# Kernel tuning notes

Hardware: AMD Instinct MI355X
Metric: run time of the kernel (lower is better)

## Reference

```python
import jax, jax.numpy as jnp
import numpy as np

N = 20000
E = 640000
H, C = 4, 64
L = 3
B = 16
EPS = 1e-5


def setup_inputs() -> dict:
    key = jax.random.key(0)
    ks = jax.random.split(key, 12)
    x = jax.random.normal(ks[0], (N, 256), dtype=jnp.float32)
    edge_index = jax.random.randint(ks[1], (2, E), 0, N, dtype=jnp.int64)
    batch = jnp.sort(jax.random.randint(ks[2], (N,), 0, B, dtype=jnp.int64))
    s = 0.05
    return {
        "x": x,
        "edge_index": edge_index,
        "batch": batch,
        "Wl": jax.random.normal(ks[3], (L, 256, H * C), dtype=jnp.float32) * s,
        "bl": jnp.zeros((L, H * C), dtype=jnp.float32),
        "Wr": jax.random.normal(ks[4], (L, 256, H * C), dtype=jnp.float32) * s,
        "br": jnp.zeros((L, H * C), dtype=jnp.float32),
        "att": jax.random.normal(ks[5], (L, H, C), dtype=jnp.float32) * s,
        "conv_bias": jnp.zeros((L, H * C), dtype=jnp.float32),
        "prelu_a": jnp.full((L,), 0.25, dtype=jnp.float32),
        "norm_w": jnp.ones((H * C,), dtype=jnp.float32),
        "norm_b": jnp.zeros((H * C,), dtype=jnp.float32),
        "norm_alpha": jnp.ones((H * C,), dtype=jnp.float32),
        "fc_W": jax.random.normal(ks[6], (H * C, 128), dtype=jnp.float32) * s,
        "fc_b": jnp.zeros((128,), dtype=jnp.float32),
    }


def graph_norm(h, w, b, alpha):
    # GraphNorm with batch=None: all rows form one segment (as in source forward)
    mean = jnp.mean(h, axis=0, keepdims=True)
    shifted = h - alpha * mean
    var = jnp.mean(shifted * shifted, axis=0, keepdims=True)
    return w * shifted / jnp.sqrt(var + EPS) + b


def gatv2_layer(h, src, dst, Wl, bl, Wr, br, att, bias):
    xl = (h @ Wl + bl).reshape(N, H, C)  # source transform
    xr = (h @ Wr + br).reshape(N, H, C)  # target transform
    m = jax.nn.leaky_relu(xl[src] + xr[dst], negative_slope=0.2)  # [Etot,H,C]
    e = jnp.einsum("ehc,hc->eh", m, att)  # [Etot,H]
    emax = jax.ops.segment_max(e, dst, num_segments=N)  # self-loops guarantee coverage
    ex = jnp.exp(e - emax[dst])
    denom = jax.ops.segment_sum(ex, dst, num_segments=N)
    alpha = ex / denom[dst]
    out = jax.ops.segment_sum(alpha[:, :, None] * xl[src], dst, num_segments=N)
    return out.reshape(N, H * C) + bias


def reference(x, edge_index, batch, Wl, bl, Wr, br, att, conv_bias, prelu_a,
              norm_w, norm_b, norm_alpha, fc_W, fc_b):
    loop = jnp.arange(N, dtype=edge_index.dtype)
    src = jnp.concatenate([edge_index[0], loop])  # add self-loops (PyG default)
    dst = jnp.concatenate([edge_index[1], loop])
    h = x
    for l in range(L):
        h = gatv2_layer(h, src, dst, Wl[l], bl[l], Wr[l], br[l], att[l], conv_bias[l])
        h = graph_norm(h, norm_w, norm_b, norm_alpha)
        h = jnp.where(h >= 0, h, prelu_a[l] * h)  # PReLU; dropout is identity in eval
    pooled = jax.ops.segment_sum(h, batch, num_segments=B)  # global_add_pool
    pooled = graph_norm(pooled, norm_w, norm_b, norm_alpha)  # shared norm reused after pool
    return pooled @ fc_W + fc_b
```

## Files before the change

### kernel.cpp

```cpp
#include <hip/hip_runtime.h>
#include <math.h>

#define N_NODES 20000
#define N_EDGES 640000
#define ETOT (N_EDGES + N_NODES)
#define HC 256
#define NLAYER 3
#define NBATCH 16
#define GEPS 1e-5f
#define NSLOT 64
#define L2E 1.44269504f

typedef unsigned short u16;
typedef unsigned int u32;
typedef __attribute__((ext_vector_type(8))) short short8;
typedef __attribute__((ext_vector_type(4))) float floatx4;

__device__ __forceinline__ u16 f2bf(float f) {
    u32 u = __float_as_uint(f);
    u32 r = (u + 0x7FFFu + ((u >> 16) & 1u)) >> 16;
    return (u16)r;
}

__device__ __forceinline__ float4 bf2f4(uint2 u) {
    float4 r;
    r.x = __uint_as_float(u.x << 16);
    r.y = __uint_as_float(u.x & 0xFFFF0000u);
    r.z = __uint_as_float(u.y << 16);
    r.w = __uint_as_float(u.y & 0xFFFF0000u);
    return r;
}

__device__ __forceinline__ float dpp_red16(float x) {
    x += __int_as_float(__builtin_amdgcn_update_dpp(0, __float_as_int(x), 0xB1, 0xF, 0xF, true));
    x += __int_as_float(__builtin_amdgcn_update_dpp(0, __float_as_int(x), 0x4E, 0xF, 0xF, true));
    x += __int_as_float(__builtin_amdgcn_update_dpp(0, __float_as_int(x), 0x141, 0xF, 0xF, true));
    x += __int_as_float(__builtin_amdgcn_update_dpp(0, __float_as_int(x), 0x140, 0xF, 0xF, true));
    return x;
}


__global__ __launch_bounds__(256) void prep(const float* __restrict__ x, u16* __restrict__ xbf,
                                            const float* __restrict__ Wl, const float* __restrict__ Wr,
                                            u16* __restrict__ WT, uint4* __restrict__ zbase, int zq) {
    int b = blockIdx.x, tid = threadIdx.x;
    if (b < 1000) {
        for (int i = b * 256 + tid; i < 640000; i += 256000) {
            const float4* x4 = (const float4*)x + (size_t)i * 2;
            float4 a = x4[0], c = x4[1];
            u16 o[8] = {f2bf(a.x), f2bf(a.y), f2bf(a.z), f2bf(a.w),
                        f2bf(c.x), f2bf(c.y), f2bf(c.z), f2bf(c.w)};
            ((uint4*)xbf)[i] = *(const uint4*)o;
        }
    } else if (b < 1384) {
        __shared__ float T[32][33];
        int bi = b - 1000;
        int kb = bi & 7, nbk = (bi >> 3) & 15, l = bi >> 7;
        int n0 = nbk * 32, k0 = kb * 32;
        const float* W = ((n0 < 256) ? Wl : Wr) + (size_t)l * 65536;
        int nn = n0 & 255;
        int tx = tid & 31, ty = tid >> 5;
        #pragma unroll
        for (int i = 0; i < 4; ++i)
            T[ty + i * 8][tx] = W[(size_t)(k0 + ty + i * 8) * 256 + nn + tx];
        __syncthreads();
        u16* outw = WT + (size_t)l * 512 * 256;
        #pragma unroll
        for (int i = 0; i < 4; ++i)
            outw[(size_t)(n0 + ty + i * 8) * 256 + k0 + tx] = f2bf(T[tx][ty + i * 8]);
    } else {
        uint4 z = make_uint4(0, 0, 0, 0);
        for (int i = (b - 1384) * 256 + tid; i < zq; i += 120 * 256) zbase[i] = z;
    }
}


__global__ void count_deg(const int* __restrict__ dst, int* __restrict__ deg) {
    int e = blockIdx.x * 256 + threadIdx.x;
    if (e < N_EDGES) atomicAdd(&deg[dst[e]], 1);
}

__global__ __launch_bounds__(1024) void scan_excl(int* __restrict__ data, int* __restrict__ cursor) {
    __shared__ int wsum[16];
    int t = threadIdx.x, lane = t & 63, wid = t >> 6;
    int i0 = t * 20;
    int d[20];
    int tot = 0;
    #pragma unroll
    for (int j = 0; j < 20; ++j) {
        int i = i0 + j;
        int v = (i < N_NODES) ? (data[i] + 1) : 0;
        d[j] = v;
        tot += v;
    }
    int x = tot;
    #pragma unroll
    for (int off = 1; off < 64; off <<= 1) {
        int tmp = __shfl_up(x, off);
        if (lane >= off) x += tmp;
    }
    if (lane == 63) wsum[wid] = x;
    __syncthreads();
    if (t == 0) {
        int run = 0;
        #pragma unroll
        for (int w = 0; w < 16; ++w) { int tv = wsum[w]; wsum[w] = run; run += tv; }
    }
    __syncthreads();
    int run = wsum[wid] + x - tot;
    #pragma unroll
    for (int j = 0; j < 20; ++j) {
        int i = i0 + j;
        if (i < N_NODES) { data[i] = run; cursor[i] = run; }
        run += d[j];
    }
    if (t == 0) data[N_NODES] = ETOT;
}

__global__ void scatter_edges(const int* __restrict__ src, const int* __restrict__ dst,
                              int* __restrict__ cursor, int* __restrict__ col) {
    int t = blockIdx.x * 256 + threadIdx.x;
    if (t < N_NODES) {
        int p = atomicAdd(&cursor[t], 1);
        col[p] = t;
    } else if (t < N_NODES + N_EDGES) {
        int e = t - N_NODES;
        int p = atomicAdd(&cursor[dst[e]], 1);
        col[p] = src[e];
    }
}


__global__ __launch_bounds__(256) void gemm_mfma(
    const u16* __restrict__ Abf, const u16* __restrict__ WT3,
    const float* __restrict__ b0, const float* __restrict__ b1,
    u16* __restrict__ xlb, u16* __restrict__ xrb) {
    int row0 = blockIdx.x * 128;
    int strip = blockIdx.y;
    const float* bias = (strip < 2) ? b0 : b1;
    u16* outp = (strip < 2) ? xlb : xrb;
    int c0 = (strip & 1) * 128;
    const u16* Wbase = WT3 + (size_t)strip * 128 * 256;

    int tid = threadIdx.x;
    int wave = tid >> 6, lane = tid & 63;
    int wm = (wave & 1) * 64, wn = (wave >> 1) * 64;
    int quad = lane >> 4, l16 = lane & 15;

    floatx4 acc[4][4] = {};
    const u16* pA[4];
    const u16* pB[4];
    #pragma unroll
    for (int mi = 0; mi < 4; ++mi) {
        int r = row0 + wm + mi * 16 + l16;
        r = min(r, N_NODES - 1);
        pA[mi] = Abf + (size_t)r * 256 + quad * 8;
    }
    #pragma unroll
    for (int ni = 0; ni < 4; ++ni)
        pB[ni] = Wbase + (size_t)(wn + ni * 16 + l16) * 256 + quad * 8;

    #pragma unroll 2
    for (int k0 = 0; k0 < 256; k0 += 32) {
        short8 af[4], bf[4];
        #pragma unroll
        for (int mi = 0; mi < 4; ++mi) af[mi] = *(const short8*)(pA[mi] + k0);
        #pragma unroll
        for (int ni = 0; ni < 4; ++ni) bf[ni] = *(const short8*)(pB[ni] + k0);
        #pragma unroll
        for (int mi = 0; mi < 4; ++mi)
            #pragma unroll
            for (int ni = 0; ni < 4; ++ni)
                acc[mi][ni] = __builtin_amdgcn_mfma_f32_16x16x32_bf16(af[mi], bf[ni], acc[mi][ni], 0, 0, 0);
    }

    #pragma unroll
    for (int ni = 0; ni < 4; ++ni) {
        int col = c0 + wn + ni * 16 + l16;
        float bv = bias[col];
        #pragma unroll
        for (int mi = 0; mi < 4; ++mi) {
            int gr = row0 + wm + mi * 16 + quad * 4;
            #pragma unroll
            for (int r = 0; r < 4; ++r) {
                if (gr + r < N_NODES)
                    outp[(size_t)(gr + r) * 256 + col] = f2bf(acc[mi][ni][r] + bv);
            }
        }
    }
}


__global__ __launch_bounds__(256) void gat_agg(
    const u16* __restrict__ xlb, const u16* __restrict__ xrb,
    const int* __restrict__ rowptr, const int* __restrict__ col,
    const float* __restrict__ att_l, const float* __restrict__ bias_l,
    u16* __restrict__ hB, float* __restrict__ slot) {
    __shared__ float sred[4][520];
    int wid = threadIdx.x >> 6, lane = threadIdx.x & 63;
    int node = blockIdx.x * 4 + wid;
    const uint2* xl2 = (const uint2*)xlb;
    float4 attv = ((const float4*)att_l)[lane];
    attv.x *= L2E; attv.y *= L2E; attv.z *= L2E; attv.w *= L2E;
    float4 xrv = bf2f4(((const uint2*)xrb)[(size_t)node * 64 + lane]);
    int beg = rowptr[node], end = rowptr[node + 1];

    float denom = 0.f;
    float4 acc = make_float4(0.f, 0.f, 0.f, 0.f);

    int j = beg;
    for (; j + 8 <= end; j += 8) {
        int s[8];
        uint2 raw[8];
        float4 a[8];
        float p[8];
        #pragma unroll
        for (int u = 0; u < 8; ++u) s[u] = col[j + u];
        #pragma unroll
        for (int u = 0; u < 8; ++u) raw[u] = xl2[(size_t)s[u] * 64 + lane];
        #pragma unroll
        for (int u = 0; u < 8; ++u) {
            a[u] = bf2f4(raw[u]);
            float vx = a[u].x + xrv.x, vy = a[u].y + xrv.y;
            float vz = a[u].z + xrv.z, vw = a[u].w + xrv.w;
            vx = fmaxf(vx, 0.2f * vx);
            vy = fmaxf(vy, 0.2f * vy);
            vz = fmaxf(vz, 0.2f * vz);
            vw = fmaxf(vw, 0.2f * vw);
            p[u] = vx * attv.x + vy * attv.y + vz * attv.z + vw * attv.w;
        }
        #pragma unroll
        for (int u = 0; u < 8; ++u) p[u] = dpp_red16(p[u]);
        #pragma unroll
        for (int u = 0; u < 8; ++u) {
            float w = exp2f(p[u]);
            denom += w;
            acc.x += w * a[u].x; acc.y += w * a[u].y;
            acc.z += w * a[u].z; acc.w += w * a[u].w;
        }
    }
    for (; j < end; ++j) {
        int s = col[j];
        float4 a = bf2f4(xl2[(size_t)s * 64 + lane]);
        float vx = a.x + xrv.x, vy = a.y + xrv.y;
        float vz = a.z + xrv.z, vw = a.w + xrv.w;
        vx = fmaxf(vx, 0.2f * vx);
        vy = fmaxf(vy, 0.2f * vy);
        vz = fmaxf(vz, 0.2f * vz);
        vw = fmaxf(vw, 0.2f * vw);
        float p = vx * attv.x + vy * attv.y + vz * attv.z + vw * attv.w;
        p = dpp_red16(p);
        float w = exp2f(p);
        denom += w;
        acc.x += w * a.x; acc.y += w * a.y; acc.z += w * a.z; acc.w += w * a.w;
    }

    float inv = 1.f / denom;
    float4 b4 = ((const float4*)bias_l)[lane];
    float4 o;
    o.x = acc.x * inv + b4.x; o.y = acc.y * inv + b4.y;
    o.z = acc.z * inv + b4.z; o.w = acc.w * inv + b4.w;
    u16 ob[4] = {f2bf(o.x), f2bf(o.y), f2bf(o.z), f2bf(o.w)};
    ((uint2*)hB)[(size_t)node * 64 + lane] = *(const uint2*)ob;

    int cb2 = lane * 4;
    sred[wid][cb2 + 0] = o.x; sred[wid][cb2 + 1] = o.y;
    sred[wid][cb2 + 2] = o.z; sred[wid][cb2 + 3] = o.w;
    sred[wid][256 + cb2 + 0] = o.x * o.x; sred[wid][256 + cb2 + 1] = o.y * o.y;
    sred[wid][256 + cb2 + 2] = o.z * o.z; sred[wid][256 + cb2 + 3] = o.w * o.w;
    __syncthreads();
    int t = threadIdx.x;
    #pragma unroll
    for (int h = 0; h < 2; ++h) {
        int idx = t + h * 256;
        float s = sred[0][idx] + sred[1][idx] + sred[2][idx] + sred[3][idx];
        atomicAdd(&slot[(blockIdx.x & (NSLOT - 1)) * 512 + idx], s);
    }
}


__global__ __launch_bounds__(256) void fin_stats(const float* __restrict__ slot,
                                                 const float* __restrict__ nw, const float* __restrict__ nb,
                                                 const float* __restrict__ na,
                                                 float* __restrict__ wcbb) {
    int c = threadIdx.x;
    float sum = 0.f, sq = 0.f;
    for (int s = 0; s < NSLOT; ++s) {
        sum += slot[s * 512 + c];
        sq += slot[s * 512 + 256 + c];
    }
    const float invn = 1.f / (float)N_NODES;
    float mean = sum * invn, Eh2 = sq * invn;
    float a = na[c];
    float var = Eh2 - (2.f * a - a * a) * mean * mean;
    float wc = nw[c] * rsqrtf(var + GEPS);
    wcbb[c] = wc;
    wcbb[256 + c] = nb[c] - a * mean * wc;
}


__global__ __launch_bounds__(256) void norm_prelu(const u16* __restrict__ hB, u16* __restrict__ hbf,
                                                  const float* __restrict__ wcbb,
                                                  const float* __restrict__ pa, int l) {
    int t = threadIdx.x;
    int row = blockIdx.x * 8 + (t >> 5);
    int c = (t & 31) * 8;
    float ap = pa[l];
    float4 wc0 = *(const float4*)&wcbb[c];
    float4 wc1 = *(const float4*)&wcbb[c + 4];
    float4 bb0 = *(const float4*)&wcbb[256 + c];
    float4 bb1 = *(const float4*)&wcbb[256 + c + 4];
    uint4 raw = ((const uint4*)hB)[(size_t)row * 32 + (c >> 3)];
    float4 a = bf2f4(make_uint2(raw.x, raw.y));
    float4 b = bf2f4(make_uint2(raw.z, raw.w));
    a.x = a.x * wc0.x + bb0.x; a.y = a.y * wc0.y + bb0.y;
    a.z = a.z * wc0.z + bb0.z; a.w = a.w * wc0.w + bb0.w;
    b.x = b.x * wc1.x + bb1.x; b.y = b.y * wc1.y + bb1.y;
    b.z = b.z * wc1.z + bb1.z; b.w = b.w * wc1.w + bb1.w;
    a.x = fmaxf(a.x, ap * a.x); a.y = fmaxf(a.y, ap * a.y);
    a.z = fmaxf(a.z, ap * a.z); a.w = fmaxf(a.w, ap * a.w);
    b.x = fmaxf(b.x, ap * b.x); b.y = fmaxf(b.y, ap * b.y);
    b.z = fmaxf(b.z, ap * b.z); b.w = fmaxf(b.w, ap * b.w);
    u16 o[8] = {f2bf(a.x), f2bf(a.y), f2bf(a.z), f2bf(a.w),
                f2bf(b.x), f2bf(b.y), f2bf(b.z), f2bf(b.w)};
    ((uint4*)hbf)[(size_t)row * 32 + (c >> 3)] = *(const uint4*)o;
}


__global__ __launch_bounds__(256) void pool_kernel(const u16* __restrict__ hB,
                                                   const int* __restrict__ batch,
                                                   const float* __restrict__ slots2,
                                                   const float* __restrict__ nw, const float* __restrict__ nb,
                                                   const float* __restrict__ na, const float* __restrict__ pa,
                                                   float* __restrict__ pooled) {
    __shared__ float accs[NBATCH][256];
    int c = threadIdx.x;
    float sum = 0.f, sq = 0.f;
    for (int s = 0; s < NSLOT; ++s) {
        sum += slots2[s * 512 + c];
        sq += slots2[s * 512 + 256 + c];
    }
    const float invn = 1.f / (float)N_NODES;
    float mean = sum * invn, Eh2 = sq * invn;
    float a = na[c];
    float var = Eh2 - (2.f * a - a * a) * mean * mean;
    float wc = nw[c] * rsqrtf(var + GEPS);
    float bb = nb[c] - a * mean * wc;
    float ap = pa[2];

    #pragma unroll
    for (int b = 0; b < NBATCH; ++b) accs[b][c] = 0.f;
    int r0 = blockIdx.x * 100;
    int r1 = min(N_NODES, r0 + 100);
    for (int i = r0; i < r1; ++i) {
        float v = __uint_as_float(((u32)hB[(size_t)i * 256 + c]) << 16);
        v = v * wc + bb;
        v = fmaxf(v, ap * v);
        accs[batch[i]][c] += v;
    }
    int bmin = batch[r0], bmax = batch[r1 - 1];
    for (int b = bmin; b <= bmax; ++b) atomicAdd(&pooled[b * 256 + c], accs[b][c]);
}


__global__ __launch_bounds__(256) void pool_norm(const float* __restrict__ pooled,
                                                 const float* __restrict__ nw, const float* __restrict__ nb,
                                                 const float* __restrict__ na,
                                                 float* __restrict__ pn) {
    int c = threadIdx.x;
    float mean = 0.f, sq = 0.f;
    #pragma unroll
    for (int i = 0; i < NBATCH; ++i) {
        float v = pooled[i * 256 + c];
        mean += v; sq += v * v;
    }
    mean *= (1.f / NBATCH); sq *= (1.f / NBATCH);
    float a = na[c];
    float var = sq - (2.f * a - a * a) * mean * mean;
    float wc = nw[c] * rsqrtf(var + GEPS);
    float bb = nb[c] - a * mean * wc;
    #pragma unroll
    for (int i = 0; i < NBATCH; ++i)
        pn[i * 256 + c] = pooled[i * 256 + c] * wc + bb;
}


__global__ __launch_bounds__(256) void fc_kernel(const float* __restrict__ pn,
                                                 const float* __restrict__ fcW, const float* __restrict__ fcb,
                                                 float* __restrict__ out) {
    __shared__ float pnl[256];
    __shared__ float part[128];
    int b = blockIdx.x;
    int t = threadIdx.x;
    pnl[t] = pn[b * 256 + t];
    __syncthreads();
    int o = t & 127, half = t >> 7;
    float s = 0.f;
    int kbase = half * 128;
    #pragma unroll 8
    for (int k = 0; k < 128; ++k)
        s += pnl[kbase + k] * fcW[(kbase + k) * 128 + o];
    if (half == 1) part[o] = s;
    __syncthreads();
    if (half == 0) out[b * 128 + o] = s + part[o] + fcb[o];
}


extern "C" void kernel_launch(void* const* d_in, const int* in_sizes, int n_in,
                              void* d_out, int out_size, void* d_ws, size_t ws_size,
                              hipStream_t stream) {
    const float* x    = (const float*)d_in[0];
    const int*   ei   = (const int*)d_in[1];
    const int*   batch= (const int*)d_in[2];
    const float* Wl   = (const float*)d_in[3];
    const float* bl   = (const float*)d_in[4];
    const float* Wr   = (const float*)d_in[5];
    const float* br   = (const float*)d_in[6];
    const float* att  = (const float*)d_in[7];
    const float* cb   = (const float*)d_in[8];
    const float* pa   = (const float*)d_in[9];
    const float* nw   = (const float*)d_in[10];
    const float* nb   = (const float*)d_in[11];
    const float* na   = (const float*)d_in[12];
    const float* fcW  = (const float*)d_in[13];
    const float* fcb  = (const float*)d_in[14];
    float* out = (float*)d_out;

    char* ws = (char*)d_ws;
    size_t off = 0;
    auto carve = [&](size_t bytes) -> void* {
        void* p = (void*)(ws + off);
        off += (bytes + 255) & ~(size_t)255;
        return p;
    };
    size_t z0 = off;
    int*   rowptr = (int*)carve((N_NODES + 1) * sizeof(int));
    float* slots  = (float*)carve((size_t)NLAYER * NSLOT * 512 * sizeof(float));
    float* pooled = (float*)carve(NBATCH * HC * sizeof(float));
    size_t z1 = off;
    int*   cursor = (int*)carve(N_NODES * sizeof(int));
    int*   colidx = (int*)carve((size_t)ETOT * sizeof(int));
    u16*   xlb    = (u16*)carve((size_t)N_NODES * HC * sizeof(u16));
    u16*   xrb    = (u16*)carve((size_t)N_NODES * HC * sizeof(u16));
    u16*   hB     = (u16*)carve((size_t)N_NODES * HC * sizeof(u16));
    u16*   xbf    = (u16*)carve((size_t)N_NODES * HC * sizeof(u16));
    u16*   hbf    = (u16*)carve((size_t)N_NODES * HC * sizeof(u16));
    u16*   WT     = (u16*)carve((size_t)NLAYER * 512 * 256 * sizeof(u16));
    float* wcbb   = (float*)carve(512 * sizeof(float));
    float* pn     = (float*)carve(NBATCH * HC * sizeof(float));

    int zq = (int)((z1 - z0) / 16);
    const int* srcp = ei;
    const int* dstp = ei + N_EDGES;

    prep<<<1504, 256, 0, stream>>>(x, xbf, Wl, Wr, WT, (uint4*)(ws + z0), zq);
    count_deg<<<(N_EDGES + 255) / 256, 256, 0, stream>>>(dstp, rowptr);
    scan_excl<<<1, 1024, 0, stream>>>(rowptr, cursor);
    scatter_edges<<<(ETOT + 255) / 256, 256, 0, stream>>>(srcp, dstp, cursor, colidx);

    for (int l = 0; l < NLAYER; ++l) {
        const u16* Asrc = (l == 0) ? xbf : hbf;
        gemm_mfma<<<dim3(157, 4), 256, 0, stream>>>(Asrc, WT + (size_t)l * 512 * 256,
                                                    bl + l * 256, br + l * 256, xlb, xrb);
        gat_agg<<<5000, 256, 0, stream>>>(xlb, xrb, rowptr, colidx, att + l * 256, cb + l * 256,
                                          hB, slots + (size_t)l * NSLOT * 512);
        if (l < NLAYER - 1) {
            fin_stats<<<1, 256, 0, stream>>>(slots + (size_t)l * NSLOT * 512, nw, nb, na, wcbb);
            norm_prelu<<<2500, 256, 0, stream>>>(hB, hbf, wcbb, pa, l);
        }
    }
    pool_kernel<<<200, 256, 0, stream>>>(hB, batch, slots + (size_t)2 * NSLOT * 512,
                                         nw, nb, na, pa, pooled);
    pool_norm<<<1, 256, 0, stream>>>(pooled, nw, nb, na, pn);
    fc_kernel<<<NBATCH, 256, 0, stream>>>(pn, fcW, fcb, out);
}
```

Before: 532.3 us.

## Pre-tile GEMM operands into MFMA fragment layout, split edge aggregation, fuse final kernels

The producers of the GEMM inputs (x conversion, weight transpose, norm_prelu) now write bf16 data in a tiled layout matching the MFMA 16x32 fragment order. Each lane of gemm_mfma then loads a contiguous 16-byte chunk, which removes strided row loads. gat_agg now uses two waves per node, each handling half of the edge list, and combines their partial softmax sums and accumulators through shared memory to expose more memory-level parallelism. pool_norm and fc are fused into one kernel to save a launch. The costs are an extra block-wide sync in gat_agg and a less readable layout.

```diff
diff --git a/kernel.cpp b/kernel.cpp
--- a/kernel.cpp
+++ b/kernel.cpp
@@ -40,37 +40,51 @@
 }
 
 
+
 __global__ __launch_bounds__(256) void prep(const float* __restrict__ x, u16* __restrict__ xbf,
                                             const float* __restrict__ Wl, const float* __restrict__ Wr,
                                             u16* __restrict__ WT, uint4* __restrict__ zbase, int zq) {
+    __shared__ float T[32][33];
     int b = blockIdx.x, tid = threadIdx.x;
-    if (b < 1000) {
-        for (int i = b * 256 + tid; i < 640000; i += 256000) {
-            const float4* x4 = (const float4*)x + (size_t)i * 2;
-            float4 a = x4[0], c = x4[1];
+    if (b < 1250) {
+        int rt = b;
+        int wid = tid >> 6, lane = tid & 63;
+        int row = rt * 16 + (lane & 15);
+        int q8 = (lane >> 4) * 8;
+        #pragma unroll
+        for (int kk = 0; kk < 2; ++kk) {
+            int kt = wid + kk * 4;
+            int kcol = kt * 32 + q8;
+            const float4* px = (const float4*)(x + (size_t)row * 256 + kcol);
+            float4 a = px[0], c = px[1];
             u16 o[8] = {f2bf(a.x), f2bf(a.y), f2bf(a.z), f2bf(a.w),
                         f2bf(c.x), f2bf(c.y), f2bf(c.z), f2bf(c.w)};
-            ((uint4*)xbf)[i] = *(const uint4*)o;
+            *(uint4*)(xbf + (((size_t)rt * 8 + kt) * 64 + lane) * 8) = *(const uint4*)o;
         }
-    } else if (b < 1384) {
-        __shared__ float T[32][33];
-        int bi = b - 1000;
-        int kb = bi & 7, nbk = (bi >> 3) & 15, l = bi >> 7;
-        int n0 = nbk * 32, k0 = kb * 32;
+    } else if (b < 1634) {
+        int bi = b - 1250;
+        int kb = bi & 7;
+        int nb = (bi >> 3) & 15;
+        int l = bi >> 7;
+        int n0 = nb * 32, k0 = kb * 32;
         const float* W = ((n0 < 256) ? Wl : Wr) + (size_t)l * 65536;
-        int nn = n0 & 255;
+        int nn0 = n0 & 255;
         int tx = tid & 31, ty = tid >> 5;
         #pragma unroll
         for (int i = 0; i < 4; ++i)
-            T[ty + i * 8][tx] = W[(size_t)(k0 + ty + i * 8) * 256 + nn + tx];
+            T[ty + i * 8][tx] = W[(size_t)(k0 + ty + i * 8) * 256 + nn0 + tx];
         __syncthreads();
-        u16* outw = WT + (size_t)l * 512 * 256;
-        #pragma unroll
-        for (int i = 0; i < 4; ++i)
-            outw[(size_t)(n0 + ty + i * 8) * 256 + k0 + tx] = f2bf(T[tx][ty + i * 8]);
+        int lane = tid & 63, jp = (tid >> 6) & 1, cl = tid >> 7;
+        int ct = n0 / 16 + cl;
+        u16 o4[4];
+        #pragma unroll
+        for (int jj = 0; jj < 4; ++jj)
+            o4[jj] = f2bf(T[(lane >> 4) * 8 + jp * 4 + jj][cl * 16 + (lane & 15)]);
+        u16* outw = WT + (size_t)l * 131072;
+        *(uint2*)(outw + (((size_t)ct * 8 + kb) * 64 + lane) * 8 + jp * 4) = *(const uint2*)o4;
     } else {
         uint4 z = make_uint4(0, 0, 0, 0);
-        for (int i = (b - 1384) * 256 + tid; i < zq; i += 120 * 256) zbase[i] = z;
+        for (int i = (b - 1634) * 256 + tid; i < zq; i += 120 * 256) zbase[i] = z;
     }
 }
 
@@ -132,7 +146,7 @@
 
 
 __global__ __launch_bounds__(256) void gemm_mfma(
-    const u16* __restrict__ Abf, const u16* __restrict__ WT3,
+    const u16* __restrict__ At, const u16* __restrict__ WTt,
     const float* __restrict__ b0, const float* __restrict__ b1,
     u16* __restrict__ xlb, u16* __restrict__ xrb) {
     int row0 = blockIdx.x * 128;
@@ -140,33 +154,33 @@
     const float* bias = (strip < 2) ? b0 : b1;
     u16* outp = (strip < 2) ? xlb : xrb;
     int c0 = (strip & 1) * 128;
-    const u16* Wbase = WT3 + (size_t)strip * 128 * 256;
 
     int tid = threadIdx.x;
     int wave = tid >> 6, lane = tid & 63;
     int wm = (wave & 1) * 64, wn = (wave >> 1) * 64;
     int quad = lane >> 4, l16 = lane & 15;
+    int rt0 = (row0 + wm) >> 4;
+    int ct0 = (strip * 128 + wn) >> 4;
 
     floatx4 acc[4][4] = {};
     const u16* pA[4];
     const u16* pB[4];
     #pragma unroll
     for (int mi = 0; mi < 4; ++mi) {
-        int r = row0 + wm + mi * 16 + l16;
-        r = min(r, N_NODES - 1);
-        pA[mi] = Abf + (size_t)r * 256 + quad * 8;
+        int rt = min(rt0 + mi, 1249);
+        pA[mi] = At + ((size_t)rt * 8) * 512 + lane * 8;
     }
     #pragma unroll
     for (int ni = 0; ni < 4; ++ni)
-        pB[ni] = Wbase + (size_t)(wn + ni * 16 + l16) * 256 + quad * 8;
-
-    #pragma unroll 2
-    for (int k0 = 0; k0 < 256; k0 += 32) {
+        pB[ni] = WTt + ((size_t)(ct0 + ni) * 8) * 512 + lane * 8;
+
+    #pragma unroll
+    for (int kt = 0; kt < 8; ++kt) {
         short8 af[4], bf[4];
         #pragma unroll
-        for (int mi = 0; mi < 4; ++mi) af[mi] = *(const short8*)(pA[mi] + k0);
-        #pragma unroll
-        for (int ni = 0; ni < 4; ++ni) bf[ni] = *(const short8*)(pB[ni] + k0);
+        for (int mi = 0; mi < 4; ++mi) af[mi] = *(const short8*)(pA[mi] + kt * 512);
+        #pragma unroll
+        for (int ni = 0; ni < 4; ++ni) bf[ni] = *(const short8*)(pB[ni] + kt * 512);
         #pragma unroll
         for (int mi = 0; mi < 4; ++mi)
             #pragma unroll
@@ -191,25 +205,31 @@
 }
 
 
-__global__ __launch_bounds__(256) void gat_agg(
+__global__ __launch_bounds__(512) void gat_agg(
     const u16* __restrict__ xlb, const u16* __restrict__ xrb,
     const int* __restrict__ rowptr, const int* __restrict__ col,
     const float* __restrict__ att_l, const float* __restrict__ bias_l,
     u16* __restrict__ hB, float* __restrict__ slot) {
+    __shared__ float pden[8][64];
+    __shared__ float4 pacc[8][64];
     __shared__ float sred[4][520];
     int wid = threadIdx.x >> 6, lane = threadIdx.x & 63;
-    int node = blockIdx.x * 4 + wid;
+    int nw = wid >> 1, half = wid & 1;
+    int node = blockIdx.x * 4 + nw;
     const uint2* xl2 = (const uint2*)xlb;
     float4 attv = ((const float4*)att_l)[lane];
     attv.x *= L2E; attv.y *= L2E; attv.z *= L2E; attv.w *= L2E;
     float4 xrv = bf2f4(((const uint2*)xrb)[(size_t)node * 64 + lane]);
     int beg = rowptr[node], end = rowptr[node + 1];
+    int mid = (beg + end) >> 1;
+    int j0 = half ? mid : beg;
+    int j1 = half ? end : mid;
 
     float denom = 0.f;
     float4 acc = make_float4(0.f, 0.f, 0.f, 0.f);
 
-    int j = beg;
-    for (; j + 8 <= end; j += 8) {
+    int j = j0;
+    for (; j + 8 <= j1; j += 8) {
         int s[8];
         uint2 raw[8];
         float4 a[8];
@@ -239,7 +259,7 @@
             acc.z += w * a[u].z; acc.w += w * a[u].w;
         }
     }
-    for (; j < end; ++j) {
+    for (; j < j1; ++j) {
         int s = col[j];
         float4 a = bf2f4(xl2[(size_t)s * 64 + lane]);
         float vx = a.x + xrv.x, vy = a.y + xrv.y;
@@ -255,27 +275,32 @@
         acc.x += w * a.x; acc.y += w * a.y; acc.z += w * a.z; acc.w += w * a.w;
     }
 
-    float inv = 1.f / denom;
-    float4 b4 = ((const float4*)bias_l)[lane];
-    float4 o;
-    o.x = acc.x * inv + b4.x; o.y = acc.y * inv + b4.y;
-    o.z = acc.z * inv + b4.z; o.w = acc.w * inv + b4.w;
-    u16 ob[4] = {f2bf(o.x), f2bf(o.y), f2bf(o.z), f2bf(o.w)};
-    ((uint2*)hB)[(size_t)node * 64 + lane] = *(const uint2*)ob;
-
-    int cb2 = lane * 4;
-    sred[wid][cb2 + 0] = o.x; sred[wid][cb2 + 1] = o.y;
-    sred[wid][cb2 + 2] = o.z; sred[wid][cb2 + 3] = o.w;
-    sred[wid][256 + cb2 + 0] = o.x * o.x; sred[wid][256 + cb2 + 1] = o.y * o.y;
-    sred[wid][256 + cb2 + 2] = o.z * o.z; sred[wid][256 + cb2 + 3] = o.w * o.w;
+    if (half == 1) {
+        pden[wid][lane] = denom;
+        pacc[wid][lane] = acc;
+    }
+    __syncthreads();
+    if (half == 0) {
+        denom += pden[wid + 1][lane];
+        float4 o2 = pacc[wid + 1][lane];
+        acc.x += o2.x; acc.y += o2.y; acc.z += o2.z; acc.w += o2.w;
+        float inv = 1.f / denom;
+        float4 b4 = ((const float4*)bias_l)[lane];
+        float4 o;
+        o.x = acc.x * inv + b4.x; o.y = acc.y * inv + b4.y;
+        o.z = acc.z * inv + b4.z; o.w = acc.w * inv + b4.w;
+        u16 ob[4] = {f2bf(o.x), f2bf(o.y), f2bf(o.z), f2bf(o.w)};
+        ((uint2*)hB)[(size_t)node * 64 + lane] = *(const uint2*)ob;
+        int cb2 = lane * 4;
+        sred[nw][cb2 + 0] = o.x; sred[nw][cb2 + 1] = o.y;
+        sred[nw][cb2 + 2] = o.z; sred[nw][cb2 + 3] = o.w;
+        sred[nw][256 + cb2 + 0] = o.x * o.x; sred[nw][256 + cb2 + 1] = o.y * o.y;
+        sred[nw][256 + cb2 + 2] = o.z * o.z; sred[nw][256 + cb2 + 3] = o.w * o.w;
+    }
     __syncthreads();
     int t = threadIdx.x;
-    #pragma unroll
-    for (int h = 0; h < 2; ++h) {
-        int idx = t + h * 256;
-        float s = sred[0][idx] + sred[1][idx] + sred[2][idx] + sred[3][idx];
-        atomicAdd(&slot[(blockIdx.x & (NSLOT - 1)) * 512 + idx], s);
-    }
+    float s = sred[0][t] + sred[1][t] + sred[2][t] + sred[3][t];
+    atomicAdd(&slot[(blockIdx.x & (NSLOT - 1)) * 512 + t], s);
 }
 
 
@@ -299,31 +324,37 @@
 }
 
 
-__global__ __launch_bounds__(256) void norm_prelu(const u16* __restrict__ hB, u16* __restrict__ hbf,
+__global__ __launch_bounds__(256) void norm_prelu(const u16* __restrict__ hB, u16* __restrict__ hbfT,
                                                   const float* __restrict__ wcbb,
                                                   const float* __restrict__ pa, int l) {
-    int t = threadIdx.x;
-    int row = blockIdx.x * 8 + (t >> 5);
-    int c = (t & 31) * 8;
+    int rt = blockIdx.x;
+    int wid = threadIdx.x >> 6, lane = threadIdx.x & 63;
     float ap = pa[l];
-    float4 wc0 = *(const float4*)&wcbb[c];
-    float4 wc1 = *(const float4*)&wcbb[c + 4];
-    float4 bb0 = *(const float4*)&wcbb[256 + c];
-    float4 bb1 = *(const float4*)&wcbb[256 + c + 4];
-    uint4 raw = ((const uint4*)hB)[(size_t)row * 32 + (c >> 3)];
-    float4 a = bf2f4(make_uint2(raw.x, raw.y));
-    float4 b = bf2f4(make_uint2(raw.z, raw.w));
-    a.x = a.x * wc0.x + bb0.x; a.y = a.y * wc0.y + bb0.y;
-    a.z = a.z * wc0.z + bb0.z; a.w = a.w * wc0.w + bb0.w;
-    b.x = b.x * wc1.x + bb1.x; b.y = b.y * wc1.y + bb1.y;
-    b.z = b.z * wc1.z + bb1.z; b.w = b.w * wc1.w + bb1.w;
-    a.x = fmaxf(a.x, ap * a.x); a.y = fmaxf(a.y, ap * a.y);
-    a.z = fmaxf(a.z, ap * a.z); a.w = fmaxf(a.w, ap * a.w);
-    b.x = fmaxf(b.x, ap * b.x); b.y = fmaxf(b.y, ap * b.y);
-    b.z = fmaxf(b.z, ap * b.z); b.w = fmaxf(b.w, ap * b.w);
-    u16 o[8] = {f2bf(a.x), f2bf(a.y), f2bf(a.z), f2bf(a.w),
-                f2bf(b.x), f2bf(b.y), f2bf(b.z), f2bf(b.w)};
-    ((uint4*)hbf)[(size_t)row * 32 + (c >> 3)] = *(const uint4*)o;
+    int row = rt * 16 + (lane & 15);
+    int q8 = (lane >> 4) * 8;
+    #pragma unroll
+    for (int kk = 0; kk < 2; ++kk) {
+        int kt = wid + kk * 4;
+        int kcol = kt * 32 + q8;
+        uint4 raw = *(const uint4*)(hB + (size_t)row * 256 + kcol);
+        float4 a = bf2f4(make_uint2(raw.x, raw.y));
+        float4 b = bf2f4(make_uint2(raw.z, raw.w));
+        float4 wc0 = *(const float4*)&wcbb[kcol];
+        float4 wc1 = *(const float4*)&wcbb[kcol + 4];
+        float4 bb0 = *(const float4*)&wcbb[256 + kcol];
+        float4 bb1 = *(const float4*)&wcbb[256 + kcol + 4];
+        a.x = a.x * wc0.x + bb0.x; a.y = a.y * wc0.y + bb0.y;
+        a.z = a.z * wc0.z + bb0.z; a.w = a.w * wc0.w + bb0.w;
+        b.x = b.x * wc1.x + bb1.x; b.y = b.y * wc1.y + bb1.y;
+        b.z = b.z * wc1.z + bb1.z; b.w = b.w * wc1.w + bb1.w;
+        a.x = fmaxf(a.x, ap * a.x); a.y = fmaxf(a.y, ap * a.y);
+        a.z = fmaxf(a.z, ap * a.z); a.w = fmaxf(a.w, ap * a.w);
+        b.x = fmaxf(b.x, ap * b.x); b.y = fmaxf(b.y, ap * b.y);
+        b.z = fmaxf(b.z, ap * b.z); b.w = fmaxf(b.w, ap * b.w);
+        u16 o[8] = {f2bf(a.x), f2bf(a.y), f2bf(a.z), f2bf(a.w),
+                    f2bf(b.x), f2bf(b.y), f2bf(b.z), f2bf(b.w)};
+        *(uint4*)(hbfT + (((size_t)rt * 8 + kt) * 64 + lane) * 8) = *(const uint4*)o;
+    }
 }
 
 
@@ -363,10 +394,14 @@
 }
 
 
-__global__ __launch_bounds__(256) void pool_norm(const float* __restrict__ pooled,
-                                                 const float* __restrict__ nw, const float* __restrict__ nb,
-                                                 const float* __restrict__ na,
-                                                 float* __restrict__ pn) {
+__global__ __launch_bounds__(256) void poolnorm_fc(const float* __restrict__ pooled,
+                                                   const float* __restrict__ nw, const float* __restrict__ nb,
+                                                   const float* __restrict__ na,
+                                                   const float* __restrict__ fcW, const float* __restrict__ fcb,
+                                                   float* __restrict__ out) {
+    __shared__ float pn[256];
+    __shared__ float part[128];
+    int b = blockIdx.x;
     int c = threadIdx.x;
     float mean = 0.f, sq = 0.f;
     #pragma unroll
@@ -379,27 +414,14 @@
     float var = sq - (2.f * a - a * a) * mean * mean;
     float wc = nw[c] * rsqrtf(var + GEPS);
     float bb = nb[c] - a * mean * wc;
-    #pragma unroll
-    for (int i = 0; i < NBATCH; ++i)
-        pn[i * 256 + c] = pooled[i * 256 + c] * wc + bb;
-}
-
-
-__global__ __launch_bounds__(256) void fc_kernel(const float* __restrict__ pn,
-                                                 const float* __restrict__ fcW, const float* __restrict__ fcb,
-                                                 float* __restrict__ out) {
-    __shared__ float pnl[256];
-    __shared__ float part[128];
-    int b = blockIdx.x;
-    int t = threadIdx.x;
-    pnl[t] = pn[b * 256 + t];
-    __syncthreads();
-    int o = t & 127, half = t >> 7;
+    pn[c] = pooled[b * 256 + c] * wc + bb;
+    __syncthreads();
+    int o = c & 127, half = c >> 7;
     float s = 0.f;
     int kbase = half * 128;
     #pragma unroll 8
     for (int k = 0; k < 128; ++k)
-        s += pnl[kbase + k] * fcW[(kbase + k) * 128 + o];
+        s += pn[kbase + k] * fcW[(kbase + k) * 128 + o];
     if (half == 1) part[o] = s;
     __syncthreads();
     if (half == 0) out[b * 128 + o] = s + part[o] + fcb[o];
@@ -447,30 +469,28 @@
     u16*   hbf    = (u16*)carve((size_t)N_NODES * HC * sizeof(u16));
     u16*   WT     = (u16*)carve((size_t)NLAYER * 512 * 256 * sizeof(u16));
     float* wcbb   = (float*)carve(512 * sizeof(float));
-    float* pn     = (float*)carve(NBATCH * HC * sizeof(float));
 
     int zq = (int)((z1 - z0) / 16);
     const int* srcp = ei;
     const int* dstp = ei + N_EDGES;
 
-    prep<<<1504, 256, 0, stream>>>(x, xbf, Wl, Wr, WT, (uint4*)(ws + z0), zq);
+    prep<<<1754, 256, 0, stream>>>(x, xbf, Wl, Wr, WT, (uint4*)(ws + z0), zq);
     count_deg<<<(N_EDGES + 255) / 256, 256, 0, stream>>>(dstp, rowptr);
     scan_excl<<<1, 1024, 0, stream>>>(rowptr, cursor);
     scatter_edges<<<(ETOT + 255) / 256, 256, 0, stream>>>(srcp, dstp, cursor, colidx);
 
     for (int l = 0; l < NLAYER; ++l) {
         const u16* Asrc = (l == 0) ? xbf : hbf;
-        gemm_mfma<<<dim3(157, 4), 256, 0, stream>>>(Asrc, WT + (size_t)l * 512 * 256,
+        gemm_mfma<<<dim3(157, 4), 256, 0, stream>>>(Asrc, WT + (size_t)l * 131072,
                                                     bl + l * 256, br + l * 256, xlb, xrb);
-        gat_agg<<<5000, 256, 0, stream>>>(xlb, xrb, rowptr, colidx, att + l * 256, cb + l * 256,
+        gat_agg<<<5000, 512, 0, stream>>>(xlb, xrb, rowptr, colidx, att + l * 256, cb + l * 256,
                                           hB, slots + (size_t)l * NSLOT * 512);
         if (l < NLAYER - 1) {
             fin_stats<<<1, 256, 0, stream>>>(slots + (size_t)l * NSLOT * 512, nw, nb, na, wcbb);
-            norm_prelu<<<2500, 256, 0, stream>>>(hB, hbf, wcbb, pa, l);
+            norm_prelu<<<1250, 256, 0, stream>>>(hB, hbf, wcbb, pa, l);
         }
     }
     pool_kernel<<<200, 256, 0, stream>>>(hB, batch, slots + (size_t)2 * NSLOT * 512,
                                          nw, nb, na, pa, pooled);
-    pool_norm<<<1, 256, 0, stream>>>(pooled, nw, nb, na, pn);
-    fc_kernel<<<NBATCH, 256, 0, stream>>>(pn, fcW, fcb, out);
-}
+    poolnorm_fc<<<16, 256, 0, stream>>>(pooled, nw, nb, na, fcW, fcb, out);
+}
```

Result: slower. 548.1 us (+3.0%).
